# Optimization experiments

Measured on AMD Instinct MI355X. Metric: run time of the kernel, lower is better.

Reference implementation:

```python
import jax, jax.numpy as jnp
import numpy as np

DIM = 512
BATCH = 256
LOG_2PI = float(np.log(2.0 * np.pi))


def setup_inputs() -> dict:
    key = jax.random.key(0)
    k_x, k_mu, k_ld, k_lt, k_m = jax.random.split(key, 5)
    n_tril = DIM * (DIM - 1) // 2  # 130816
    x = jax.random.normal(k_x, (BATCH, DIM), dtype=jnp.float32)
    mu = jax.random.normal(k_mu, (DIM,), dtype=jnp.float32)
    log_diagonal = jax.random.normal(k_ld, (DIM,), dtype=jnp.float32)
    # scale strict-lower entries for reasonable conditioning of cov = A A^T
    lower_tri = jax.random.normal(k_lt, (n_tril,), dtype=jnp.float32) * 0.05
    mask = jax.random.randint(k_m, (BATCH, DIM), 0, 2) > 0
    return {"x": x, "mu": mu, "log_diagonal": log_diagonal,
            "lower_tri": lower_tri, "mask": mask}


def _build_cov(log_diagonal, lower_tri):
    D = log_diagonal.shape[0]
    ti, tj = np.tril_indices(D, -1)
    A = jnp.zeros((D, D), dtype=log_diagonal.dtype).at[ti, tj].set(lower_tri)
    A = A + jnp.diag(jnp.exp(log_diagonal))
    return A @ A.T  # SPD covariance [D, D]


def reference(x, mu, log_diagonal, lower_tri, mask):
    cov = _build_cov(log_diagonal, lower_tri)          # [D, D]
    m = mask.astype(x.dtype)                           # [B, D]
    D = cov.shape[0]
    # Block-diagonalized masked covariance: observed block = cov[m][:,m],
    # unobserved block = identity. Equivalent to per-sample submatrix gather.
    cov_m = (m[:, :, None] * m[:, None, :]) * cov[None] \
            + jnp.eye(D, dtype=x.dtype)[None] * (1.0 - m)[:, :, None]  # [B, D, D]
    L = jnp.linalg.cholesky(cov_m)                     # batched [B, D, D]
    r = (x - mu) * m                                   # masked residual [B, D]
    z = jax.scipy.linalg.solve_triangular(L, r[..., None], lower=True)[..., 0]
    quad = jnp.sum(z * z, axis=-1)                     # [B]
    # unobserved diag of L is 1 -> contributes 0 to logdet
    logdet = 2.0 * jnp.sum(jnp.log(jnp.diagonal(L, axis1=-2, axis2=-1)), axis=-1)
    d_obs = jnp.sum(m, axis=-1)
    return 0.5 * (quad + logdet + d_obs * LOG_2PI)     # neg log prob, [B]
```

## Files before the change

kernel.cpp:

```cpp
#include <hip/hip_runtime.h>
#include <hip/hip_bf16.h>

#define LOG_2PI 1.8378770664093453f
#define R0 256
#define GSTRIDE 512
#define TRI_FLOATS 33280
#define CSTR 68
#define NT 256
#define SMEM_FLOATS (TRI_FLOATS + 512 + 512 + 512 + 16 + 64*CSTR)
#define SMEM_BYTES (SMEM_FLOATS * 4)

__device__ __forceinline__ int tribase(int r) {
    int m = r & 3;
    return r * (r + 1) / 2 + 6 * (r >> 2) + ((m * (7 - m)) >> 1);
}

__global__ __launch_bounds__(256) void build_A(const float* __restrict__ logd,
                                               const float* __restrict__ lt,
                                               float* __restrict__ A) {
    int idx = blockIdx.x * 256 + threadIdx.x;
    int i = idx >> 9, j = idx & 511;
    float v;
    if (j < i)       v = lt[(i * (i - 1)) / 2 + j];
    else if (j == i) v = expf(logd[i]);
    else             v = 0.f;
    A[idx] = v;
}

__global__ __launch_bounds__(256) void aat(const float* __restrict__ A,
                                           float* __restrict__ C) {
    __shared__ float Ash[32][33];
    __shared__ float Bsh[32][33];
    int tx = threadIdx.x & 31, ty = threadIdx.x >> 5;
    int bi = blockIdx.y, bj = blockIdx.x;
    float acc[4] = {0.f, 0.f, 0.f, 0.f};
    for (int k0 = 0; k0 < 512; k0 += 32) {
        #pragma unroll
        for (int q = 0; q < 4; q++) {
            int r = ty + q * 8;
            Ash[r][tx] = A[(bi * 32 + r) * 512 + k0 + tx];
            Bsh[r][tx] = A[(bj * 32 + r) * 512 + k0 + tx];
        }
        __syncthreads();
        for (int c = 0; c < 32; c++) {
            float bv = Bsh[tx][c];
            #pragma unroll
            for (int q = 0; q < 4; q++) acc[q] += Ash[ty + q * 8][c] * bv;
        }
        __syncthreads();
    }
    #pragma unroll
    for (int q = 0; q < 4; q++)
        C[(bi * 32 + ty + q * 8) * 512 + bj * 32 + tx] = acc[q];
}

__global__ __launch_bounds__(256) void compact(const float* __restrict__ x,
                                               const float* __restrict__ mu,
                                               const int* __restrict__ mask,
                                               int* __restrict__ obs_idx,
                                               int* __restrict__ n_obs,
                                               float* __restrict__ rc) {
    int b = blockIdx.x, t = threadIdx.x;
    __shared__ int wsum[4];
    int i0 = 2 * t, i1 = 2 * t + 1;
    int m0 = (mask[b * 512 + i0] != 0) ? 1 : 0;
    int m1 = (mask[b * 512 + i1] != 0) ? 1 : 0;
    int local = m0 + m1;
    int v = local;
    int lane = t & 63, wv = t >> 6;
    #pragma unroll
    for (int off = 1; off < 64; off <<= 1) {
        int u = __shfl_up(v, off, 64);
        if (lane >= off) v += u;
    }
    if (lane == 63) wsum[wv] = v;
    __syncthreads();
    int woff = 0;
    for (int w = 0; w < wv; w++) woff += wsum[w];
    int excl = woff + v - local;
    if (m0) { obs_idx[b * 512 + excl] = i0; rc[b * 512 + excl] = x[b * 512 + i0] - mu[i0]; }
    if (m1) { int p = excl + m0; obs_idx[b * 512 + p] = i1; rc[b * 512 + p] = x[b * 512 + i1] - mu[i1]; }
    if (t == 0) n_obs[b] = wsum[0] + wsum[1] + wsum[2] + wsum[3];
}

template <typename RPF>
__device__ __forceinline__ void diag_block(RPF rptr, float* zsh, float* dinvAll,
                                           float& llog, int j0, int nb, int n, int tid) {
    if (tid < 32) {
        int l = tid;
        int r = j0 + l;
        float a[32];
        float z = 0.f;
        if (r < n) {
            const float4* src = (const float4*)(rptr(r) + j0);
            #pragma unroll
            for (int q = 0; q < 8; q++) {
                float4 t = src[q];
                a[4*q+0] = t.x; a[4*q+1] = t.y; a[4*q+2] = t.z; a[4*q+3] = t.w;
            }
            z = zsh[r];
        } else {
            #pragma unroll
            for (int q = 0; q < 32; q++) a[q] = 0.f;
        }
        float dv = 0.f;
        #pragma unroll
        for (int k = 0; k < 32; k++) {
            if (k < nb) {
                float akk = __shfl(a[k], k, 64);
                float rin = rsqrtf(akk);
                float lkk = akk * rin;
                if (l == k) { dv = rin; llog += __logf(lkk); }
                a[k] = (l == k) ? lkk : a[k] * rin;
                #pragma unroll
                for (int j = k + 1; j < 32; j++) {
                    float ajk = __shfl(a[k], j, 64);
                    a[j] -= a[k] * ajk;
                }
            }
        }
        #pragma unroll
        for (int k = 0; k < 32; k++) {
            if (k < nb) {
                if (l == k) z *= dv;
                float zk = __shfl(z, k, 64);
                if (l > k) z -= a[k] * zk;
            }
        }
        dinvAll[j0 + l] = dv;
        if (l < nb) {
            zsh[r] = z;
            float* dst = rptr(r) + j0;
            #pragma unroll
            for (int c = 0; c < 32; c++)
                if (c <= l) dst[c] = a[c];
        }
    }
}

__device__ __forceinline__ void syrk_macro32(float* T, int rbase0, int cbase0,
                                             int j0, int n0, int lane, bool diag) {
    int ty = lane >> 3, tx = lane & 7;
    int rbase = rbase0 + ty * 4, cbase = cbase0 + tx * 4;
    if (diag && cbase > rbase + 3) return;
    int ra[4], rb[4];
    #pragma unroll
    for (int a = 0; a < 4; a++) {
        ra[a] = tribase(min(rbase + a, n0 - 1)) + j0;
        rb[a] = tribase(min(cbase + a, n0 - 1)) + j0;
    }
    float acc[4][4];
    #pragma unroll
    for (int a = 0; a < 4; a++)
        #pragma unroll
        for (int c = 0; c < 4; c++) acc[a][c] = 0.f;
    #pragma unroll
    for (int q = 0; q < 8; q++) {
        float4 av[4], bv[4];
        #pragma unroll
        for (int a = 0; a < 4; a++) av[a] = *(const float4*)&T[ra[a] + 4 * q];
        #pragma unroll
        for (int c = 0; c < 4; c++) bv[c] = *(const float4*)&T[rb[c] + 4 * q];
        #pragma unroll
        for (int a = 0; a < 4; a++)
            #pragma unroll
            for (int c = 0; c < 4; c++)
                acc[a][c] += av[a].x*bv[c].x + av[a].y*bv[c].y +
                             av[a].z*bv[c].z + av[a].w*bv[c].w;
    }
    #pragma unroll
    for (int a = 0; a < 4; a++) {
        int r = rbase + a;
        if (r < n0) {
            float* trow = T + tribase(r);
            if (cbase + 3 <= r) {
                float4 v = *(const float4*)&trow[cbase];
                v.x -= acc[a][0]; v.y -= acc[a][1];
                v.z -= acc[a][2]; v.w -= acc[a][3];
                *(float4*)&trow[cbase] = v;
            } else {
                #pragma unroll
                for (int c = 0; c < 4; c++) {
                    int cl = cbase + c;
                    if (cl <= r) trow[cl] -= acc[a][c];
                }
            }
        }
    }
}

__global__ __launch_bounds__(NT) void chol_solve(
    const float* __restrict__ cov, const float* __restrict__ rc,
    const int* __restrict__ obs_idx, const int* __restrict__ n_obs,
    float* __restrict__ gtail_all, float* __restrict__ out) {

    extern __shared__ float smem[];
    float* T       = smem;
    float* zsh     = T + TRI_FLOATS;
    int*   oi      = (int*)(zsh + 512);
    float* dinvAll = (float*)(oi + 512);
    float* red     = dinvAll + 512;
    float* SBc     = red + 16;

    int b = blockIdx.x, tid = threadIdx.x;
    int lane = tid & 63, wv = tid >> 6;
    int n = n_obs[b]; if (n > 512) n = 512;
    float* gtail = gtail_all + (size_t)b * 256 * GSTRIDE;
    if (n == 0) { if (tid == 0) out[b] = 0.f; return; }

    for (int i = tid; i < n; i += NT) {
        oi[i] = obs_idx[b * 512 + i];
        zsh[i] = rc[b * 512 + i];
    }
    __syncthreads();

    int n0 = (n < R0) ? n : R0;
    int ntail = n - n0;

    for (int r = wv; r < n0; r += 4) {
        const float* crow = cov + (size_t)oi[r] * 512;
        float* dst = T + tribase(r);
        #pragma unroll 4
        for (int j = lane; j <= r; j += 64) dst[j] = crow[oi[j]];
    }
    for (int r = n0 + wv; r < n; r += 4) {
        const float* crow = cov + (size_t)oi[r] * 512;
        float* dst = gtail + (size_t)(r - n0) * GSTRIDE;
        #pragma unroll 4
        for (int j = lane; j < n0; j += 64) dst[j] = crow[oi[j]];
    }
    __syncthreads();

    float llog = 0.f;

    for (int j0 = 0; j0 < n0; j0 += 32) {
        int nb = min(32, n0 - j0);
        diag_block([&](int r) { return T + tribase(r); },
                   zsh, dinvAll, llog, j0, nb, n0, tid);
        __syncthreads();

        int mL = n0 - j0 - 32; if (mL < 0) mL = 0;
        int mtot = mL + ntail;
        if (mtot == 0) continue;

        {
            float dvv[32];
            #pragma unroll
            for (int q = 0; q < 8; q++) {
                float4 t4 = *(const float4*)&dinvAll[j0 + 4 * q];
                dvv[4*q+0] = t4.x; dvv[4*q+1] = t4.y;
                dvv[4*q+2] = t4.z; dvv[4*q+3] = t4.w;
            }
            for (int idx = tid; idx < mtot; idx += NT) {
                int r; float* prow;
                if (idx < mL) { r = j0 + 32 + idx; prow = T + tribase(r) + j0; }
                else          { r = n0 + (idx - mL);
                                prow = gtail + (size_t)(idx - mL) * GSTRIDE + j0; }
                float p[32];
                #pragma unroll
                for (int q = 0; q < 8; q++) {
                    float4 t = *(const float4*)&prow[4 * q];
                    p[4*q+0] = t.x; p[4*q+1] = t.y; p[4*q+2] = t.z; p[4*q+3] = t.w;
                }
                #pragma unroll
                for (int j = 0; j < 32; j++) {
                    const float* dj = T + tribase(j0 + j) + j0;
                    float s0 = 0.f, s1 = 0.f, s2 = 0.f, s3 = 0.f;
                    int jf = j >> 2;
                    for (int q2 = 0; q2 < jf; q2++) {
                        float4 t = *(const float4*)&dj[q2 * 4];
                        s0 += p[q2*4+0]*t.x; s1 += p[q2*4+1]*t.y;
                        s2 += p[q2*4+2]*t.z; s3 += p[q2*4+3]*t.w;
                    }
                    float acc = p[j] - ((s0 + s1) + (s2 + s3));
                    for (int c = jf * 4; c < j; c++) acc -= p[c] * dj[c];
                    p[j] = acc * dvv[j];
                }
                float zu = 0.f;
                #pragma unroll
                for (int q = 0; q < 8; q++) {
                    *(float4*)&prow[4 * q] = make_float4(p[4*q], p[4*q+1], p[4*q+2], p[4*q+3]);
                    float4 zz = *(const float4*)&zsh[j0 + 4 * q];
                    zu += p[4*q]*zz.x + p[4*q+1]*zz.y + p[4*q+2]*zz.z + p[4*q+3]*zz.w;
                }
                zsh[r] -= zu;
            }
        }
        __syncthreads();

        if (mL > 0) {
            int nMac = (mL + 31) >> 5;
            int pairs = nMac * (nMac + 1) / 2;
            for (int e = wv; e < pairs; e += 4) {
                int MI = 0;
                while ((MI + 1) * (MI + 2) / 2 <= e) MI++;
                int MJ = e - MI * (MI + 1) / 2;
                syrk_macro32(T, j0 + 32 + MI * 32, j0 + 32 + MJ * 32,
                             j0, n0, lane, MI == MJ);
            }
        }

        if (ntail > 0 && mL > 0) {
            int nRM = (ntail + 31) >> 5;
            int nCM = mL >> 5;
            int tot = nRM * nCM;
            int ty = lane >> 3, tx = lane & 7;
            for (int e = wv; e < tot; e += 4) {
                int MI = e / nCM, MJ = e % nCM;
                int r0 = MI * 32 + ty * 4;
                int c0 = j0 + 32 + MJ * 32 + tx * 4;
                int rb[4], tcb[4];
                #pragma unroll
                for (int a = 0; a < 4; a++) {
                    rb[a] = min(r0 + a, ntail - 1);
                    tcb[a] = tribase(min(c0 + a, n0 - 1)) + j0;
                }
                float acc[4][4];
                #pragma unroll
                for (int a = 0; a < 4; a++)
                    #pragma unroll
                    for (int c = 0; c < 4; c++) acc[a][c] = 0.f;
                #pragma unroll
                for (int q = 0; q < 8; q++) {
                    float4 av[4], bv[4];
                    #pragma unroll
                    for (int a = 0; a < 4; a++)
                        av[a] = *(const float4*)&gtail[(size_t)rb[a] * GSTRIDE + j0 + 4 * q];
                    #pragma unroll
                    for (int c = 0; c < 4; c++)
                        bv[c] = *(const float4*)&T[tcb[c] + 4 * q];
                    #pragma unroll
                    for (int a = 0; a < 4; a++)
                        #pragma unroll
                        for (int c = 0; c < 4; c++)
                            acc[a][c] += av[a].x*bv[c].x + av[a].y*bv[c].y +
                                         av[a].z*bv[c].z + av[a].w*bv[c].w;
                }
                #pragma unroll
                for (int a = 0; a < 4; a++) {
                    int r = r0 + a;
                    if (r < ntail) {
                        float* grow = gtail + (size_t)r * GSTRIDE;
                        float4 g4 = *(const float4*)&grow[c0];
                        g4.x -= acc[a][0]; g4.y -= acc[a][1];
                        g4.z -= acc[a][2]; g4.w -= acc[a][3];
                        *(float4*)&grow[c0] = g4;
                    }
                }
            }
        }
        __syncthreads();
    }

    for (int gs2 = R0; gs2 < n; gs2 += 64) {
        int t1 = min(64, n - gs2);
        int g1 = gs2 - R0;

        for (int cp = R0; cp < gs2; cp += 32) {
            if (tid < t1) {
                int r = gs2 + tid;
                float* row = gtail + (size_t)(r - R0) * GSTRIDE;
                const float* crow = cov + (size_t)oi[r] * 512;
                float zacc = 0.f;
                for (int j = 0; j < 32; j++) {
                    int jj = cp + j;
                    const float* Lrow = gtail + (size_t)(jj - R0) * GSTRIDE;
                    float s0 = 0.f, s1 = 0.f, s2 = 0.f, s3 = 0.f;
                    int jv = jj >> 2;
                    for (int c4 = 0; c4 < jv; c4++) {
                        float4 a4 = *(const float4*)&row[c4 * 4];
                        float4 b4 = *(const float4*)&Lrow[c4 * 4];
                        s0 += a4.x*b4.x; s1 += a4.y*b4.y;
                        s2 += a4.z*b4.z; s3 += a4.w*b4.w;
                    }
                    float acc = crow[oi[jj]] - ((s0 + s1) + (s2 + s3));
                    for (int c = jv * 4; c < jj; c++) acc -= row[c] * Lrow[c];
                    float wv2 = acc * dinvAll[jj];
                    row[jj] = wv2;
                    zacc += wv2 * zsh[jj];
                }
                zsh[r] -= zacc;
            }
            __syncthreads();
        }

        {
            int npair = t1 * (t1 + 1) / 2;
            for (int e = tid; e < npair; e += NT) {
                int ti = (int)((sqrtf(8.f * (float)e + 1.f) - 1.f) * 0.5f);
                while ((ti + 1) * (ti + 2) / 2 <= e) ti++;
                while (ti * (ti + 1) / 2 > e) ti--;
                int tj = e - ti * (ti + 1) / 2;
                const float* wa = gtail + (size_t)(g1 + ti) * GSTRIDE;
                const float* wb = gtail + (size_t)(g1 + tj) * GSTRIDE;
                float s0 = 0.f, s1 = 0.f, s2 = 0.f, s3 = 0.f;
                for (int k = 0; k < gs2; k += 4) {
                    float4 a4 = *(const float4*)&wa[k];
                    float4 b4 = *(const float4*)&wb[k];
                    s0 += a4.x*b4.x; s1 += a4.y*b4.y;
                    s2 += a4.z*b4.z; s3 += a4.w*b4.w;
                }
                SBc[ti * CSTR + tj] = cov[(size_t)oi[gs2 + ti] * 512 + oi[gs2 + tj]]
                                      - ((s0 + s1) + (s2 + s3));
            }
        }
        __syncthreads();

        auto crptr = [&](int r) { return SBc + (r - gs2) * CSTR - gs2; };
        diag_block(crptr, zsh, dinvAll, llog, gs2, min(32, t1), n, tid);
        __syncthreads();
        if (t1 > 32) {
            int t2 = t1 - 32;
            if (tid < t2) {
                int r = gs2 + 32 + tid;
                float* prow = SBc + (32 + tid) * CSTR;
                float p[32];
                #pragma unroll
                for (int q = 0; q < 8; q++) {
                    float4 t = *(const float4*)&prow[4 * q];
                    p[4*q+0] = t.x; p[4*q+1] = t.y; p[4*q+2] = t.z; p[4*q+3] = t.w;
                }
                #pragma unroll
                for (int j = 0; j < 32; j++) {
                    const float* dj = SBc + j * CSTR;
                    float s0 = 0.f, s1 = 0.f, s2 = 0.f, s3 = 0.f;
                    int jf = j >> 2;
                    for (int q2 = 0; q2 < jf; q2++) {
                        float4 t = *(const float4*)&dj[q2 * 4];
                        s0 += p[q2*4+0]*t.x; s1 += p[q2*4+1]*t.y;
                        s2 += p[q2*4+2]*t.z; s3 += p[q2*4+3]*t.w;
                    }
                    float acc = p[j] - ((s0 + s1) + (s2 + s3));
                    for (int c = jf * 4; c < j; c++) acc -= p[c] * dj[c];
                    p[j] = acc * dinvAll[gs2 + j];
                }
                float zu = 0.f;
                #pragma unroll
                for (int q = 0; q < 8; q++) {
                    *(float4*)&prow[4 * q] = make_float4(p[4*q], p[4*q+1], p[4*q+2], p[4*q+3]);
                    float4 zz = *(const float4*)&zsh[gs2 + 4 * q];
                    zu += p[4*q]*zz.x + p[4*q+1]*zz.y + p[4*q+2]*zz.z + p[4*q+3]*zz.w;
                }
                zsh[r] -= zu;
            }
            __syncthreads();
            int np2 = t2 * (t2 + 1) / 2;
            for (int e = tid; e < np2; e += NT) {
                int ti = (int)((sqrtf(8.f * (float)e + 1.f) - 1.f) * 0.5f);
                while ((ti + 1) * (ti + 2) / 2 <= e) ti++;
                while (ti * (ti + 1) / 2 > e) ti--;
                int tj = e - ti * (ti + 1) / 2;
                const float* wa = SBc + (32 + ti) * CSTR;
                const float* wb = SBc + (32 + tj) * CSTR;
                float s0 = 0.f, s1 = 0.f, s2 = 0.f, s3 = 0.f;
                #pragma unroll
                for (int q = 0; q < 8; q++) {
                    float4 a4 = *(const float4*)&wa[4 * q];
                    float4 b4 = *(const float4*)&wb[4 * q];
                    s0 += a4.x*b4.x; s1 += a4.y*b4.y;
                    s2 += a4.z*b4.z; s3 += a4.w*b4.w;
                }
                SBc[(32 + ti) * CSTR + 32 + tj] -= (s0 + s1) + (s2 + s3);
            }
            __syncthreads();
            diag_block(crptr, zsh, dinvAll, llog, gs2 + 32, min(32, t2), n, tid);
            __syncthreads();
        }
        if (gs2 + 64 < n) {
            for (int e = tid; e < t1 * 64; e += NT) {
                int i = e >> 6, j = e & 63;
                if (j <= i && i < t1)
                    gtail[(size_t)(g1 + i) * GSTRIDE + gs2 + j] = SBc[i * CSTR + j];
            }
            __syncthreads();
        }
    }

    float q = 0.f;
    for (int ii = tid; ii < n; ii += NT) { float zv = zsh[ii]; q += zv * zv; }
    #pragma unroll
    for (int off = 32; off; off >>= 1) {
        q    += __shfl_down(q, off, 64);
        llog += __shfl_down(llog, off, 64);
    }
    if (lane == 0) { red[wv] = q; red[8 + wv] = llog; }
    __syncthreads();
    if (tid == 0) {
        float qt = red[0] + red[1] + red[2] + red[3];
        float ls = red[8] + red[9] + red[10] + red[11];
        out[b] = 0.5f * (qt + 2.f * ls + (float)n * LOG_2PI);
    }
}

extern "C" void kernel_launch(void* const* d_in, const int* in_sizes, int n_in,
                              void* d_out, int out_size, void* d_ws, size_t ws_size,
                              hipStream_t stream) {
    const float* x    = (const float*)d_in[0];
    const float* mu   = (const float*)d_in[1];
    const float* logd = (const float*)d_in[2];
    const float* lt   = (const float*)d_in[3];
    const int*   mask = (const int*)d_in[4];
    float* out = (float*)d_out;

    char* ws = (char*)d_ws;
    float* cov     = (float*)(ws);
    float* A       = (float*)(ws + 1048576);
    int*   n_obs   = (int*)  (ws + 2097152);
    int*   obs_idx = (int*)  (ws + 2098176);
    float* rc      = (float*)(ws + 2622464);
    float* gtail   = (float*)(ws + 3146752);

    (void)hipFuncSetAttribute((const void*)chol_solve,
                              hipFuncAttributeMaxDynamicSharedMemorySize,
                              SMEM_BYTES);

    build_A<<<1024, 256, 0, stream>>>(logd, lt, A);
    dim3 g(16, 16);
    aat<<<g, 256, 0, stream>>>(A, cov);
    compact<<<256, 256, 0, stream>>>(x, mu, mask, obs_idx, n_obs, rc);
    chol_solve<<<256, NT, SMEM_BYTES, stream>>>(cov, rc, obs_idx, n_obs, gtail, out);
}
```

Measured before the change: 402.2 us.

## Fuse A construction into AAT, exploit symmetry, and fold compaction into solver

Result: slower. 436.2 us (+8.5%).

```diff
diff --git a/kernel.cpp b/kernel.cpp
--- a/kernel.cpp
+++ b/kernel.cpp
@@ -7,7 +7,7 @@
 #define TRI_FLOATS 33280
 #define CSTR 68
 #define NT 256
-#define SMEM_FLOATS (TRI_FLOATS + 512 + 512 + 512 + 16 + 64*CSTR)
+#define SMEM_FLOATS (TRI_FLOATS + 512 + 512 + 512 + 16 + 8 + 64*CSTR)
 #define SMEM_BYTES (SMEM_FLOATS * 4)
 
 __device__ __forceinline__ int tribase(int r) {
@@ -15,31 +15,32 @@
     return r * (r + 1) / 2 + 6 * (r >> 2) + ((m * (7 - m)) >> 1);
 }
 
-__global__ __launch_bounds__(256) void build_A(const float* __restrict__ logd,
-                                               const float* __restrict__ lt,
-                                               float* __restrict__ A) {
-    int idx = blockIdx.x * 256 + threadIdx.x;
-    int i = idx >> 9, j = idx & 511;
-    float v;
-    if (j < i)       v = lt[(i * (i - 1)) / 2 + j];
-    else if (j == i) v = expf(logd[i]);
-    else             v = 0.f;
-    A[idx] = v;
-}
-
-__global__ __launch_bounds__(256) void aat(const float* __restrict__ A,
+__global__ __launch_bounds__(256) void aat(const float* __restrict__ logd,
+                                           const float* __restrict__ lt,
                                            float* __restrict__ C) {
     __shared__ float Ash[32][33];
     __shared__ float Bsh[32][33];
     int tx = threadIdx.x & 31, ty = threadIdx.x >> 5;
-    int bi = blockIdx.y, bj = blockIdx.x;
+    int e = blockIdx.x;
+    int bi = 0;
+    while ((bi + 1) * (bi + 2) / 2 <= e) bi++;
+    int bj = e - bi * (bi + 1) / 2;
     float acc[4] = {0.f, 0.f, 0.f, 0.f};
     for (int k0 = 0; k0 < 512; k0 += 32) {
         #pragma unroll
         for (int q = 0; q < 4; q++) {
-            int r = ty + q * 8;
-            Ash[r][tx] = A[(bi * 32 + r) * 512 + k0 + tx];
-            Bsh[r][tx] = A[(bj * 32 + r) * 512 + k0 + tx];
+            int rA = bi * 32 + ty + q * 8, kA = k0 + tx;
+            float vA;
+            if (kA < rA)       vA = lt[(rA * (rA - 1)) / 2 + kA];
+            else if (kA == rA) vA = expf(logd[rA]);
+            else               vA = 0.f;
+            Ash[ty + q * 8][tx] = vA;
+            int rB = bj * 32 + ty + q * 8;
+            float vB;
+            if (kA < rB)       vB = lt[(rB * (rB - 1)) / 2 + kA];
+            else if (kA == rB) vB = expf(logd[rB]);
+            else               vB = 0.f;
+            Bsh[ty + q * 8][tx] = vB;
         }
         __syncthreads();
         for (int c = 0; c < 32; c++) {
@@ -50,37 +51,11 @@
         __syncthreads();
     }
     #pragma unroll
-    for (int q = 0; q < 4; q++)
-        C[(bi * 32 + ty + q * 8) * 512 + bj * 32 + tx] = acc[q];
-}
-
-__global__ __launch_bounds__(256) void compact(const float* __restrict__ x,
-                                               const float* __restrict__ mu,
-                                               const int* __restrict__ mask,
-                                               int* __restrict__ obs_idx,
-                                               int* __restrict__ n_obs,
-                                               float* __restrict__ rc) {
-    int b = blockIdx.x, t = threadIdx.x;
-    __shared__ int wsum[4];
-    int i0 = 2 * t, i1 = 2 * t + 1;
-    int m0 = (mask[b * 512 + i0] != 0) ? 1 : 0;
-    int m1 = (mask[b * 512 + i1] != 0) ? 1 : 0;
-    int local = m0 + m1;
-    int v = local;
-    int lane = t & 63, wv = t >> 6;
-    #pragma unroll
-    for (int off = 1; off < 64; off <<= 1) {
-        int u = __shfl_up(v, off, 64);
-        if (lane >= off) v += u;
-    }
-    if (lane == 63) wsum[wv] = v;
-    __syncthreads();
-    int woff = 0;
-    for (int w = 0; w < wv; w++) woff += wsum[w];
-    int excl = woff + v - local;
-    if (m0) { obs_idx[b * 512 + excl] = i0; rc[b * 512 + excl] = x[b * 512 + i0] - mu[i0]; }
-    if (m1) { int p = excl + m0; obs_idx[b * 512 + p] = i1; rc[b * 512 + p] = x[b * 512 + i1] - mu[i1]; }
-    if (t == 0) n_obs[b] = wsum[0] + wsum[1] + wsum[2] + wsum[3];
+    for (int q = 0; q < 4; q++) {
+        int i = bi * 32 + ty + q * 8, j = bj * 32 + tx;
+        C[(size_t)i * 512 + j] = acc[q];
+        if (bi != bj) C[(size_t)j * 512 + i] = acc[q];
+    }
 }
 
 template <typename RPF>
@@ -190,8 +165,8 @@
 }
 
 __global__ __launch_bounds__(NT) void chol_solve(
-    const float* __restrict__ cov, const float* __restrict__ rc,
-    const int* __restrict__ obs_idx, const int* __restrict__ n_obs,
+    const float* __restrict__ cov, const float* __restrict__ x,
+    const float* __restrict__ mu, const int* __restrict__ mask,
     float* __restrict__ gtail_all, float* __restrict__ out) {
 
     extern __shared__ float smem[];
@@ -200,19 +175,36 @@
     int*   oi      = (int*)(zsh + 512);
     float* dinvAll = (float*)(oi + 512);
     float* red     = dinvAll + 512;
-    float* SBc     = red + 16;
+    int*   csh     = (int*)(red + 16);
+    float* SBc     = (float*)(csh + 8);
 
     int b = blockIdx.x, tid = threadIdx.x;
     int lane = tid & 63, wv = tid >> 6;
-    int n = n_obs[b]; if (n > 512) n = 512;
     float* gtail = gtail_all + (size_t)b * 256 * GSTRIDE;
+
+    {
+        int i0 = 2 * tid, i1 = 2 * tid + 1;
+        int m0 = (mask[b * 512 + i0] != 0) ? 1 : 0;
+        int m1 = (mask[b * 512 + i1] != 0) ? 1 : 0;
+        int local = m0 + m1;
+        int v = local;
+        #pragma unroll
+        for (int off = 1; off < 64; off <<= 1) {
+            int u = __shfl_up(v, off, 64);
+            if (lane >= off) v += u;
+        }
+        if (lane == 63) csh[wv] = v;
+        __syncthreads();
+        int woff = 0;
+        for (int w = 0; w < wv; w++) woff += csh[w];
+        int excl = woff + v - local;
+        if (m0) { oi[excl] = i0; zsh[excl] = x[b * 512 + i0] - mu[i0]; }
+        if (m1) { int p = excl + m0; oi[p] = i1; zsh[p] = x[b * 512 + i1] - mu[i1]; }
+        if (tid == 0) csh[4] = csh[0] + csh[1] + csh[2] + csh[3];
+        __syncthreads();
+    }
+    int n = csh[4]; if (n > 512) n = 512;
     if (n == 0) { if (tid == 0) out[b] = 0.f; return; }
-
-    for (int i = tid; i < n; i += NT) {
-        oi[i] = obs_idx[b * 512 + i];
-        zsh[i] = rc[b * 512 + i];
-    }
-    __syncthreads();
 
     int n0 = (n < R0) ? n : R0;
     int ntail = n - n0;
@@ -503,20 +495,13 @@
     float* out = (float*)d_out;
 
     char* ws = (char*)d_ws;
-    float* cov     = (float*)(ws);
-    float* A       = (float*)(ws + 1048576);
-    int*   n_obs   = (int*)  (ws + 2097152);
-    int*   obs_idx = (int*)  (ws + 2098176);
-    float* rc      = (float*)(ws + 2622464);
-    float* gtail   = (float*)(ws + 3146752);
+    float* cov   = (float*)(ws);
+    float* gtail = (float*)(ws + 1048576);
 
     (void)hipFuncSetAttribute((const void*)chol_solve,
                               hipFuncAttributeMaxDynamicSharedMemorySize,
                               SMEM_BYTES);
 
-    build_A<<<1024, 256, 0, stream>>>(logd, lt, A);
-    dim3 g(16, 16);
-    aat<<<g, 256, 0, stream>>>(A, cov);
-    compact<<<256, 256, 0, stream>>>(x, mu, mask, obs_idx, n_obs, rc);
-    chol_solve<<<256, NT, SMEM_BYTES, stream>>>(cov, rc, obs_idx, n_obs, gtail, out);
+    aat<<<136, 256, 0, stream>>>(logd, lt, cov);
+    chol_solve<<<256, NT, SMEM_BYTES, stream>>>(cov, x, mu, mask, gtail, out);
 }
```
